# Kernel tuning notes

Measured on AMD Instinct MI355X. Metric: run time of the kernel, lower is better.

Reference implementation:

```python
import jax, jax.numpy as jnp
import numpy as np

DIM = 1024
NUM_HEADS = 16
HEAD_DIM = DIM // NUM_HEADS
WINDOW = 1024
GATE_IN = 20
B, T = 2, 2048
ROPE_BASE = 10000.0


def setup_inputs() -> dict:
    key = jax.random.key(0)
    ks = jax.random.split(key, 12)
    s = 0.02
    x = jax.random.normal(ks[0], (B, T, DIM), dtype=jnp.float32)
    Wq = jax.random.normal(ks[1], (DIM, DIM), dtype=jnp.float32) * s
    bq = jnp.zeros((DIM,), jnp.float32)
    Wk = jax.random.normal(ks[2], (DIM, DIM), dtype=jnp.float32) * s
    bk = jnp.zeros((DIM,), jnp.float32)
    Wv = jax.random.normal(ks[3], (DIM, DIM), dtype=jnp.float32) * s
    bv = jnp.zeros((DIM,), jnp.float32)
    # o_lin.weight is zero-initialized in the original; use random here so the
    # reference output/grads are non-degenerate.
    Wo = jax.random.normal(ks[4], (DIM, DIM), dtype=jnp.float32) * s
    bo = jnp.zeros((DIM,), jnp.float32)
    Wg = jax.random.normal(ks[5], (NUM_HEADS, GATE_IN), dtype=jnp.float32) * s
    bg = jnp.zeros((NUM_HEADS,), jnp.float32)
    # rotary tables, half-dim convention
    inv_freq = 1.0 / (ROPE_BASE ** (jnp.arange(0, HEAD_DIM, 2, dtype=jnp.float32) / HEAD_DIM))
    t = jnp.arange(T, dtype=jnp.float32)
    freqs = jnp.outer(t, inv_freq)  # [T, HEAD_DIM/2]
    return {"x": x, "Wq": Wq, "bq": bq, "Wk": Wk, "bk": bk, "Wv": Wv, "bv": bv,
            "Wo": Wo, "bo": bo, "Wg": Wg, "bg": bg,
            "cos": jnp.cos(freqs), "sin": jnp.sin(freqs)}


def _rope(u, cos, sin):
    # u: [B,T,H,hd]; cos/sin: [T, hd/2]
    u1, u2 = jnp.split(u, 2, axis=-1)
    c = cos[None, :, None, :]
    s = sin[None, :, None, :]
    return jnp.concatenate([u1 * c - u2 * s, u1 * s + u2 * c], axis=-1)


def reference(x, Wq, bq, Wk, bk, Wv, bv, Wo, bo, Wg, bg, cos, sin):
    Bx, Tx, D = x.shape
    q = (x @ Wq.T + bq).reshape(Bx, Tx, NUM_HEADS, HEAD_DIM)
    k = (x @ Wk.T + bk).reshape(Bx, Tx, NUM_HEADS, HEAD_DIM)
    v = (x @ Wv.T + bv).reshape(Bx, Tx, NUM_HEADS, HEAD_DIM)
    q = _rope(q, cos, sin)
    k = _rope(k, cos, sin)
    scale = 1.0 / jnp.sqrt(jnp.float32(HEAD_DIM))
    scores = jnp.einsum('bqhd,bkhd->bhqk', q, k) * scale  # [B,H,T,T]
    i = jnp.arange(Tx)[:, None]
    j = jnp.arange(Tx)[None, :]
    mask = (j <= i) & (j >= i - WINDOW)  # causal + sliding window (WINDOW left, 0 right)
    scores = jnp.where(mask[None, None], scores, jnp.float32(-1e30))
    probs = jax.nn.softmax(scores, axis=-1)
    o = jnp.einsum('bhqk,bkhd->bqhd', probs, v)  # [B,T,H,hd]
    gate = jax.nn.sigmoid(x[..., :GATE_IN] @ Wg.T + bg)  # [B,T,H]
    o = o * gate[..., None]
    o = o.reshape(Bx, Tx, D)
    return o @ Wo.T + bo
```

## Files before the change

### kernel.cpp

```cpp
#include <hip/hip_runtime.h>

#define DIMM 1024
#define NHEADS 16
#define HDIM 64
#define WIN 1024
#define GATEIN 20
#define BB 2
#define TT 2048
#define MTOT (BB*TT)

typedef __attribute__((ext_vector_type(8))) short short8;
typedef __attribute__((ext_vector_type(4))) float f32x4;
typedef __attribute__((ext_vector_type(16))) float f32x16;
typedef const __attribute__((address_space(1))) void gvoid_t;
typedef __attribute__((address_space(3))) void lvoid_t;

__device__ __forceinline__ unsigned short f2b(float f) {
  union { float f; unsigned u; } c; c.f = f;
  unsigned u = c.u + 0x7fffu + ((c.u >> 16) & 1u);
  return (unsigned short)(u >> 16);
}
__device__ __forceinline__ float b2f(unsigned short s) {
  union { unsigned u; float f; } c; c.u = ((unsigned)s) << 16;
  return c.f;
}
__device__ __forceinline__ unsigned cvt_pk_bf16(float lo, float hi) {
  unsigned r;
  asm("v_cvt_pk_bf16_f32 %0, %1, %2" : "=v"(r) : "v"(lo), "v"(hi));
  return r;
}
__device__ __forceinline__ float max3f(float a, float b, float c) {
  return fmaxf(fmaxf(a, b), c);
}
__device__ __forceinline__ float xmax32(float x) {
  union { float f; unsigned u; } c; c.f = x;
  auto pr = __builtin_amdgcn_permlane32_swap(c.u, c.u, false, false);
  union { unsigned u; float f; } a, b; a.u = pr[0]; b.u = pr[1];
  return fmaxf(a.f, b.f);
}
__device__ __forceinline__ float xsum32(float x) {
  union { float f; unsigned u; } c; c.f = x;
  auto pr = __builtin_amdgcn_permlane32_swap(c.u, c.u, false, false);
  union { unsigned u; float f; } a, b; a.u = pr[0]; b.u = pr[1];
  return a.f + b.f;
}

#define QSCALE (0.125f * 1.4426950408889634f)

__global__ void prep_kernel(const float* __restrict__ x,  const float* __restrict__ Wq,
                            const float* __restrict__ Wk, const float* __restrict__ Wv,
                            const float* __restrict__ Wo, const float* __restrict__ bq,
                            const float* __restrict__ bk, const float* __restrict__ bv,
                            unsigned short* __restrict__ xb, unsigned short* __restrict__ wqkv,
                            unsigned short* __restrict__ wob, float* __restrict__ bcat) {
  int i = blockIdx.x * blockDim.x + threadIdx.x;
  const float* src; unsigned short* dst; int off;
  if (i < 1048576)      { src = x;  dst = xb;             off = i; }
  else if (i < 1310720) { src = Wq; dst = wqkv;           off = i - 1048576; }
  else if (i < 1572864) { src = Wk; dst = wqkv + 1048576; off = i - 1310720; }
  else if (i < 1835008) { src = Wv; dst = wqkv + 2097152; off = i - 1572864; }
  else if (i < 2097152) { src = Wo; dst = wob;            off = i - 1835008; }
  else {
    int j = i - 2097152;
    if (j < 768) {
      const float* bsrc = (j < 256) ? bq : (j < 512) ? bk : bv;
      int bo = (j & 255) * 4;
      int db = (j < 256) ? 0 : (j < 512) ? 1024 : 2048;
      *(float4*)(bcat + db + bo) = *(const float4*)(bsrc + bo);
    }
    return;
  }
  float4 v = ((const float4*)src)[off];
  union { unsigned short s[4]; uint2 u; } o;
  o.s[0] = f2b(v.x); o.s[1] = f2b(v.y); o.s[2] = f2b(v.z); o.s[3] = f2b(v.w);
  *(uint2*)(dst + (size_t)off * 4) = o.u;
}

__global__ void gate_kernel(const float* __restrict__ x, const float* __restrict__ Wg,
                            const float* __restrict__ bg, float* __restrict__ gate) {
  int i = blockIdx.x * blockDim.x + threadIdx.x;
  if (i >= MTOT * NHEADS) return;
  int h = i & 15;
  int m = i >> 4;
  const float* xr = x + (size_t)m * DIMM;
  const float* wr = Wg + h * GATEIN;
  float z = bg[h];
#pragma unroll
  for (int g = 0; g < GATEIN; ++g) z += xr[g] * wr[g];
  gate[i] = 1.f / (1.f + __expf(-z));
}

__global__ __launch_bounds__(256) void gemm_qkv(const unsigned short* __restrict__ A,
                                                const unsigned short* __restrict__ Bw,
                                                const float* __restrict__ bias,
                                                const float* __restrict__ cosb,
                                                const float* __restrict__ sinb,
                                                unsigned short* __restrict__ qr,
                                                unsigned short* __restrict__ kr,
                                                unsigned short* __restrict__ vt) {
  const int K = DIMM, N = 3072;
  __shared__ __align__(16) unsigned short As[2][128 * 32];
  __shared__ __align__(16) unsigned short Bs[2][128 * 32];
  const int tid = threadIdx.x;
  const int lane = tid & 63, wid = tid >> 6;
  const int g = lane >> 4, r16 = lane & 15;

  const int fid = blockIdx.y * 24 + blockIdx.x;
  const int xcd = fid & 7;
  const int j = fid >> 3;
  const int m0 = (j & 31) * 128;
  const int n0 = (xcd * 3 + (j >> 5)) * 128;

  const int wr = (wid >> 1) * 64, wc = (wid & 1) * 64;
  const int wbase = wid * 64;

  int oaf[4], obf[4];
#pragma unroll
  for (int mf = 0; mf < 4; ++mf) {
    int row = wr + mf * 16 + r16;
    oaf[mf] = row * 32 + ((g ^ ((row >> 1) & 3)) * 8);
  }
#pragma unroll
  for (int nf = 0; nf < 4; ++nf) {
    int row = wc + nf * 16 + r16;
    obf[nf] = row * 32 + ((g ^ ((row >> 1) & 3)) * 8);
  }

  f32x4 acc[4][4];
#pragma unroll
  for (int i = 0; i < 4; ++i)
#pragma unroll
    for (int j2 = 0; j2 < 4; ++j2) acc[i][j2] = (f32x4){0.f, 0.f, 0.f, 0.f};

  auto stage = [&](int buf, int k0) {
#pragma unroll
    for (int jj = 0; jj < 2; ++jj) {
      int sbase = jj * 256 + wbase;
      int s = sbase + lane;
      int l = s ^ ((s >> 3) & 3);
      const unsigned short* gA = A + (size_t)(m0 + (l >> 2)) * K + k0 + (l & 3) * 8;
      __builtin_amdgcn_global_load_lds((gvoid_t*)gA,
          (lvoid_t*)((char*)&As[buf][0] + sbase * 16), 16, 0, 0);
      const unsigned short* gB = Bw + (size_t)(n0 + (l >> 2)) * K + k0 + (l & 3) * 8;
      __builtin_amdgcn_global_load_lds((gvoid_t*)gB,
          (lvoid_t*)((char*)&Bs[buf][0] + sbase * 16), 16, 0, 0);
    }
  };

  const int NT = K >> 5;
  stage(0, 0);
  __syncthreads();
  for (int t = 0; t < NT; ++t) {
    const int buf = t & 1;
    if (t + 1 < NT) stage(buf ^ 1, (t + 1) << 5);
    short8 af[4], bf[4];
#pragma unroll
    for (int mf = 0; mf < 4; ++mf) af[mf] = *(const short8*)(&As[buf][0] + oaf[mf]);
#pragma unroll
    for (int nf = 0; nf < 4; ++nf)  bf[nf] = *(const short8*)(&Bs[buf][0] + obf[nf]);
#pragma unroll
    for (int mf = 0; mf < 4; ++mf)
#pragma unroll
      for (int nf = 0; nf < 4; ++nf)
        acc[mf][nf] = __builtin_amdgcn_mfma_f32_16x16x32_bf16(af[mf], bf[nf], acc[mf][nf], 0, 0, 0);
    __syncthreads();
  }

  const int ncol = n0 + wc;
  const int seg  = ncol >> 10;
  const int h    = (ncol >> 6) & 15;
  const int bb   = m0 >> 11;
  const int tb   = (m0 + wr) & 2047;
  const size_t base = (size_t)(bb * NHEADS + h) * TT * HDIM;
  float bias_v[4];
#pragma unroll
  for (int nf = 0; nf < 4; ++nf) bias_v[nf] = bias[ncol + nf * 16 + r16];

  if (seg == 2) {
#pragma unroll
    for (int mf = 0; mf < 4; ++mf) {
      int kvt = (tb >> 5) + (mf >> 1);
#pragma unroll
      for (int nf = 0; nf < 4; ++nf) {
        union { unsigned short s4[4]; uint2 u; } w;
#pragma unroll
        for (int rr = 0; rr < 4; ++rr) w.s4[rr] = f2b(acc[mf][nf][rr] + bias_v[nf]);
        size_t addr = base + (size_t)kvt * 2048
                    + (size_t)((nf >> 1) * 2 + (mf & 1)) * 512
                    + (size_t)(g >> 1) * 256
                    + (size_t)((nf & 1) * 16 + r16) * 8 + 4 * (g & 1);
        *(uint2*)(vt + addr) = w.u;
      }
    }
  } else {
#pragma unroll
    for (int mf = 0; mf < 4; ++mf) {
#pragma unroll
      for (int rr = 0; rr < 4; ++rr) {
        int t = tb + mf * 16 + g * 4 + rr;
#pragma unroll
        for (int nf = 0; nf < 2; ++nf) {
          int d = nf * 16 + r16;
          float c = cosb[t * 32 + d], s = sinb[t * 32 + d];
          float v1 = acc[mf][nf][rr]     + bias_v[nf];
          float v2 = acc[mf][nf + 2][rr] + bias_v[nf + 2];
          float o1 = v1 * c - v2 * s;
          float o2 = v1 * s + v2 * c;
          if (seg == 0) {
            qr[base + (size_t)t * HDIM + d]      = f2b(o1 * QSCALE);
            qr[base + (size_t)t * HDIM + d + 32] = f2b(o2 * QSCALE);
          } else {
            size_t ok = base + (size_t)(t >> 5) * 2048 + (size_t)nf * 512
                      + (size_t)(r16 >> 3) * 256 + (size_t)(t & 31) * 8 + (r16 & 7);
            kr[ok]        = f2b(o1);
            kr[ok + 1024] = f2b(o2);
          }
        }
      }
    }
  }
}

template<int MF>
__global__ __launch_bounds__(256) void gemm_bt(const unsigned short* __restrict__ A,
                                               const unsigned short* __restrict__ Bw,
                                               const float* __restrict__ bias,
                                               float* __restrict__ Cout,
                                               int M, int N, int K) {
  __shared__ __align__(16) unsigned short As[2][MF * 32 * 32];
  __shared__ __align__(16) unsigned short Bs[2][128 * 32];
  const int tid = threadIdx.x;
  const int lane = tid & 63, wid = tid >> 6;
  const int g = lane >> 4, r16 = lane & 15;
  const int m0 = blockIdx.y * (MF * 32), n0 = blockIdx.x * 128;
  const int wr = (wid >> 1) * (MF * 16), wc = (wid & 1) * 64;
  const int wbase = wid * 64;

  int oaf[MF], obf[4];
#pragma unroll
  for (int mf = 0; mf < MF; ++mf) {
    int row = wr + mf * 16 + r16;
    oaf[mf] = row * 32 + ((g ^ ((row >> 1) & 3)) * 8);
  }
#pragma unroll
  for (int nf = 0; nf < 4; ++nf) {
    int row = wc + nf * 16 + r16;
    obf[nf] = row * 32 + ((g ^ ((row >> 1) & 3)) * 8);
  }

  f32x4 acc[MF][4];
#pragma unroll
  for (int i = 0; i < MF; ++i)
#pragma unroll
    for (int j = 0; j < 4; ++j) acc[i][j] = (f32x4){0.f, 0.f, 0.f, 0.f};

  auto stage = [&](int buf, int k0) {
#pragma unroll
    for (int j = 0; j < MF / 2; ++j) {
      int sbase = j * 256 + wbase;
      int s = sbase + lane;
      int l = s ^ ((s >> 3) & 3);
      const unsigned short* gA = A + (size_t)(m0 + (l >> 2)) * K + k0 + (l & 3) * 8;
      __builtin_amdgcn_global_load_lds((gvoid_t*)gA,
          (lvoid_t*)((char*)&As[buf][0] + sbase * 16), 16, 0, 0);
    }
#pragma unroll
    for (int j = 0; j < 2; ++j) {
      int sbase = j * 256 + wbase;
      int s = sbase + lane;
      int l = s ^ ((s >> 3) & 3);
      const unsigned short* gB = Bw + (size_t)(n0 + (l >> 2)) * K + k0 + (l & 3) * 8;
      __builtin_amdgcn_global_load_lds((gvoid_t*)gB,
          (lvoid_t*)((char*)&Bs[buf][0] + sbase * 16), 16, 0, 0);
    }
  };

  const int NT = K >> 5;
  stage(0, 0);
  __syncthreads();
  for (int t = 0; t < NT; ++t) {
    const int buf = t & 1;
    if (t + 1 < NT) stage(buf ^ 1, (t + 1) << 5);
    short8 af[MF], bf[4];
#pragma unroll
    for (int mf = 0; mf < MF; ++mf) af[mf] = *(const short8*)(&As[buf][0] + oaf[mf]);
#pragma unroll
    for (int nf = 0; nf < 4; ++nf)  bf[nf] = *(const short8*)(&Bs[buf][0] + obf[nf]);
#pragma unroll
    for (int mf = 0; mf < MF; ++mf)
#pragma unroll
      for (int nf = 0; nf < 4; ++nf)
        acc[mf][nf] = __builtin_amdgcn_mfma_f32_16x16x32_bf16(af[mf], bf[nf], acc[mf][nf], 0, 0, 0);
    __syncthreads();
  }
#pragma unroll
  for (int mf = 0; mf < MF; ++mf)
#pragma unroll
    for (int nf = 0; nf < 4; ++nf)
#pragma unroll
      for (int rr = 0; rr < 4; ++rr) {
        int m = m0 + wr + mf * 16 + g * 4 + rr;
        int n = n0 + wc + nf * 16 + r16;
        Cout[(size_t)m * N + n] = acc[mf][nf][rr] + bias[n];
      }
}

__global__ __launch_bounds__(256, 4) void attn_kernel(const unsigned short* __restrict__ qr,
                                                      const unsigned short* __restrict__ kr,
                                                      const unsigned short* __restrict__ vt,
                                                      const float* __restrict__ gate,
                                                      unsigned short* __restrict__ attn_out) {
  __shared__ float lds_m[4][32];
  __shared__ float lds_l[4][32];
  __shared__ float lds_O[3][64][33];
  const int tid = threadIdx.x;
  const int lane = tid & 63, wid = tid >> 6;
  const int l31 = lane & 31, hi = lane >> 5;

  const int fid = blockIdx.x;
  const int idx = fid >> 3;
  const int bh = (fid & 7) * 4 + (idx & 3);
  const int qt = 63 - (idx >> 2);
  const int q0 = qt * 32;
  const int b = bh >> 4, h = bh & 15;
  const unsigned short* kptr = kr + (size_t)bh * TT * HDIM;
  const unsigned short* vptr = vt + (size_t)bh * TT * HDIM;
  const int q = q0 + l31;

  short8 qf[4];
#pragma unroll
  for (int st = 0; st < 4; ++st)
    qf[st] = *(const short8*)(qr + (size_t)bh * TT * HDIM + (size_t)q * HDIM + st * 16 + hi * 8);

  f32x16 o0, o1;
#pragma unroll
  for (int r = 0; r < 16; ++r) { o0[r] = 0.f; o1[r] = 0.f; }
  float mrun = -1e30f, lrun = 0.f;

  int kv_lo = q0 - WIN;
  if (kv_lo < 0) kv_lo = 0;
  const int kv_hi = q0 + 32;

  for (int kv = kv_lo + wid * 32; kv < kv_hi; kv += 128) {
    const unsigned short* kf = kptr + (size_t)kv * 64 + lane * 8;
    short8 k0 = *(const short8*)(kf);
    short8 k1 = *(const short8*)(kf + 512);
    short8 k2 = *(const short8*)(kf + 1024);
    short8 k3 = *(const short8*)(kf + 1536);

    f32x16 s;
#pragma unroll
    for (int r = 0; r < 16; ++r) s[r] = 0.f;
    s = __builtin_amdgcn_mfma_f32_32x32x16_bf16(k0, qf[0], s, 0, 0, 0);
    s = __builtin_amdgcn_mfma_f32_32x32x16_bf16(k1, qf[1], s, 0, 0, 0);
    s = __builtin_amdgcn_mfma_f32_32x32x16_bf16(k2, qf[2], s, 0, 0, 0);
    s = __builtin_amdgcn_mfma_f32_32x32x16_bf16(k3, qf[3], s, 0, 0, 0);

    if (kv == q0) {
#pragma unroll
      for (int r = 0; r < 16; ++r) {
        int key = kv + (r & 3) + 8 * (r >> 2) + 4 * hi;
        s[r] = (key <= q) ? s[r] : -1e30f;
      }
    } else if (q0 >= WIN && kv == kv_lo) {
#pragma unroll
      for (int r = 0; r < 16; ++r) {
        int key = kv + (r & 3) + 8 * (r >> 2) + 4 * hi;
        s[r] = (key + WIN >= q) ? s[r] : -1e30f;
      }
    }

    float t0 = max3f(s[0],  s[1],  s[2]);
    float t1 = max3f(s[3],  s[4],  s[5]);
    float t2 = max3f(s[6],  s[7],  s[8]);
    float t3 = max3f(s[9],  s[10], s[11]);
    float t4 = max3f(s[12], s[13], s[14]);
    float lm = fmaxf(max3f(t0, t1, t2), max3f(t3, t4, s[15]));
    lm = xmax32(lm);

    if (!__all(lm - mrun <= 8.f)) {
      float mnew = fmaxf(mrun, lm);
      float scf = __builtin_exp2f(mrun - mnew);
      mrun = mnew;
      lrun *= scf;
#pragma unroll
      for (int r = 0; r < 16; ++r) { o0[r] *= scf; o1[r] *= scf; }
    }

#pragma unroll
    for (int r = 0; r < 16; ++r) s[r] = __builtin_exp2f(s[r] - mrun);

    float c0 = (s[0] + s[1]) + (s[2] + s[3]);
    float c1 = (s[4] + s[5]) + (s[6] + s[7]);
    float c2 = (s[8] + s[9]) + (s[10] + s[11]);
    float c3 = (s[12] + s[13]) + (s[14] + s[15]);
    lrun += xsum32((c0 + c1) + (c2 + c3));

    unsigned w0 = cvt_pk_bf16(s[0],  s[1]),  w1 = cvt_pk_bf16(s[2],  s[3]);
    unsigned w2 = cvt_pk_bf16(s[4],  s[5]),  w3 = cvt_pk_bf16(s[6],  s[7]);
    unsigned w4 = cvt_pk_bf16(s[8],  s[9]),  w5 = cvt_pk_bf16(s[10], s[11]);
    unsigned w6 = cvt_pk_bf16(s[12], s[13]), w7 = cvt_pk_bf16(s[14], s[15]);
    auto s1p = __builtin_amdgcn_permlane32_swap(w0, w2, false, false);
    auto s2p = __builtin_amdgcn_permlane32_swap(w1, w3, false, false);
    auto s3p = __builtin_amdgcn_permlane32_swap(w4, w6, false, false);
    auto s4p = __builtin_amdgcn_permlane32_swap(w5, w7, false, false);
    union { unsigned u[4]; short8 s8; } pf0, pf1;
    pf0.u[0] = s1p[0]; pf0.u[1] = s2p[0]; pf0.u[2] = s1p[1]; pf0.u[3] = s2p[1];
    pf1.u[0] = s3p[0]; pf1.u[1] = s4p[0]; pf1.u[2] = s3p[1]; pf1.u[3] = s4p[1];

    const unsigned short* vf = vptr + (size_t)kv * 64 + lane * 8;
    short8 vf00 = *(const short8*)(vf);
    short8 vf01 = *(const short8*)(vf + 512);
    short8 vf10 = *(const short8*)(vf + 1024);
    short8 vf11 = *(const short8*)(vf + 1536);

    o0 = __builtin_amdgcn_mfma_f32_32x32x16_bf16(vf00, pf0.s8, o0, 0, 0, 0);
    o1 = __builtin_amdgcn_mfma_f32_32x32x16_bf16(vf10, pf0.s8, o1, 0, 0, 0);
    o0 = __builtin_amdgcn_mfma_f32_32x32x16_bf16(vf01, pf1.s8, o0, 0, 0, 0);
    o1 = __builtin_amdgcn_mfma_f32_32x32x16_bf16(vf11, pf1.s8, o1, 0, 0, 0);
  }

  if (hi == 0) { lds_m[wid][l31] = mrun; lds_l[wid][l31] = lrun; }
  __syncthreads();
  float m0 = lds_m[0][l31], m1 = lds_m[1][l31], m2 = lds_m[2][l31], m3 = lds_m[3][l31];
  float mstar = fmaxf(fmaxf(m0, m1), fmaxf(m2, m3));
  float myscale = __builtin_exp2f(mrun - mstar);
  if (wid != 0) {
#pragma unroll
    for (int r = 0; r < 16; ++r) {
      lds_O[wid - 1][lane][r]      = o0[r] * myscale;
      lds_O[wid - 1][lane][16 + r] = o1[r] * myscale;
    }
  }
  __syncthreads();
  if (wid == 0) {
    float lstar = __builtin_exp2f(m0 - mstar) * lds_l[0][l31]
                + __builtin_exp2f(m1 - mstar) * lds_l[1][l31]
                + __builtin_exp2f(m2 - mstar) * lds_l[2][l31]
                + __builtin_exp2f(m3 - mstar) * lds_l[3][l31];
    float gv = gate[((size_t)b * TT + q) * NHEADS + h];
    float inv = gv / lstar;
    float of0[16], of1[16];
#pragma unroll
    for (int r = 0; r < 16; ++r) {
      of0[r] = o0[r] * myscale + lds_O[0][lane][r]      + lds_O[1][lane][r]      + lds_O[2][lane][r];
      of1[r] = o1[r] * myscale + lds_O[0][lane][16 + r] + lds_O[1][lane][16 + r] + lds_O[2][lane][16 + r];
    }
    unsigned short* orow = attn_out + ((size_t)b * TT + q) * DIMM + h * HDIM;
#pragma unroll
    for (int a2 = 0; a2 < 4; ++a2) {
      int d0 = a2 * 8 + hi * 4;
      union { unsigned short s[4]; uint2 u; } x0, x1;
#pragma unroll
      for (int c = 0; c < 4; ++c) {
        x0.s[c] = f2b(of0[a2 * 4 + c] * inv);
        x1.s[c] = f2b(of1[a2 * 4 + c] * inv);
      }
      *(uint2*)(orow + d0) = x0.u;
      *(uint2*)(orow + 32 + d0) = x1.u;
    }
  }
}

#define OFF_XB    ((size_t)0)
#define OFF_WQKV  ((size_t)8388608)
#define OFF_WO    ((size_t)14680064)
#define OFF_BCAT  ((size_t)16777216)
#define OFF_QR    ((size_t)41959424)
#define OFF_KR    ((size_t)50348032)
#define OFF_VT    ((size_t)58736640)
#define OFF_ATTN  ((size_t)67125248)
#define OFF_GATE  ((size_t)75513856)

extern "C" void kernel_launch(void* const* d_in, const int* in_sizes, int n_in,
                              void* d_out, int out_size, void* d_ws, size_t ws_size,
                              hipStream_t stream) {
  const float* x    = (const float*)d_in[0];
  const float* Wq   = (const float*)d_in[1];
  const float* bq   = (const float*)d_in[2];
  const float* Wk   = (const float*)d_in[3];
  const float* bk   = (const float*)d_in[4];
  const float* Wv   = (const float*)d_in[5];
  const float* bv   = (const float*)d_in[6];
  const float* Wo   = (const float*)d_in[7];
  const float* bo   = (const float*)d_in[8];
  const float* Wg   = (const float*)d_in[9];
  const float* bg   = (const float*)d_in[10];
  const float* cosb = (const float*)d_in[11];
  const float* sinb = (const float*)d_in[12];
  float* out = (float*)d_out;
  char* ws = (char*)d_ws;

  unsigned short* xb    = (unsigned short*)(ws + OFF_XB);
  unsigned short* wqkv  = (unsigned short*)(ws + OFF_WQKV);
  unsigned short* wob   = (unsigned short*)(ws + OFF_WO);
  float*          bcat  = (float*)(ws + OFF_BCAT);
  unsigned short* q_r   = (unsigned short*)(ws + OFF_QR);
  unsigned short* k_r   = (unsigned short*)(ws + OFF_KR);
  unsigned short* v_t   = (unsigned short*)(ws + OFF_VT);
  unsigned short* attn  = (unsigned short*)(ws + OFF_ATTN);
  float*          gateb = (float*)(ws + OFF_GATE);

  prep_kernel<<<8195, 256, 0, stream>>>(x, Wq, Wk, Wv, Wo, bq, bk, bv, xb, wqkv, wob, bcat);
  gate_kernel<<<256, 256, 0, stream>>>(x, Wg, bg, gateb);

  gemm_qkv<<<dim3(24, 32), 256, 0, stream>>>(xb, wqkv, bcat, cosb, sinb, q_r, k_r, v_t);

  attn_kernel<<<2048, 256, 0, stream>>>(q_r, k_r, v_t, gateb, attn);

  gemm_bt<2><<<dim3(8, 64), 256, 0, stream>>>(attn, wob, bo, out, MTOT, 1024, 1024);
}
```

Before: 107.3 us.

## Split attention KV range across eight waves and drop QKV GEMM XCD swizzle

The attention kernel now launches 512 threads per block, so eight waves each take every eighth 32-key chunk of the window instead of four. The cross-wave softmax merge and LDS output reduction are widened to match, which shortens each wave's serial KV loop at the cost of more LDS and a larger final reduction done by wave 0 alone. Separately, the QKV GEMM drops its XCD-aware block remapping and uses plain blockIdx tile coordinates, which may change L2 locality across chiplets.

New measurement: 115.7 us. +7.9%, slower.

```diff
diff --git a/kernel.cpp b/kernel.cpp
--- a/kernel.cpp
+++ b/kernel.cpp
@@ -98,19 +98,13 @@
                                                 unsigned short* __restrict__ qr,
                                                 unsigned short* __restrict__ kr,
                                                 unsigned short* __restrict__ vt) {
-  const int K = DIMM, N = 3072;
+  const int K = DIMM;
   __shared__ __align__(16) unsigned short As[2][128 * 32];
   __shared__ __align__(16) unsigned short Bs[2][128 * 32];
   const int tid = threadIdx.x;
   const int lane = tid & 63, wid = tid >> 6;
   const int g = lane >> 4, r16 = lane & 15;
-
-  const int fid = blockIdx.y * 24 + blockIdx.x;
-  const int xcd = fid & 7;
-  const int j = fid >> 3;
-  const int m0 = (j & 31) * 128;
-  const int n0 = (xcd * 3 + (j >> 5)) * 128;
-
+  const int m0 = blockIdx.y * 128, n0 = blockIdx.x * 128;
   const int wr = (wid >> 1) * 64, wc = (wid & 1) * 64;
   const int wbase = wid * 64;
 
@@ -305,14 +299,14 @@
       }
 }
 
-__global__ __launch_bounds__(256, 4) void attn_kernel(const unsigned short* __restrict__ qr,
+__global__ __launch_bounds__(512, 4) void attn_kernel(const unsigned short* __restrict__ qr,
                                                       const unsigned short* __restrict__ kr,
                                                       const unsigned short* __restrict__ vt,
                                                       const float* __restrict__ gate,
                                                       unsigned short* __restrict__ attn_out) {
-  __shared__ float lds_m[4][32];
-  __shared__ float lds_l[4][32];
-  __shared__ float lds_O[3][64][33];
+  __shared__ float lds_m[8][32];
+  __shared__ float lds_l[8][32];
+  __shared__ float lds_O[7][64][33];
   const int tid = threadIdx.x;
   const int lane = tid & 63, wid = tid >> 6;
   const int l31 = lane & 31, hi = lane >> 5;
@@ -341,7 +335,7 @@
   if (kv_lo < 0) kv_lo = 0;
   const int kv_hi = q0 + 32;
 
-  for (int kv = kv_lo + wid * 32; kv < kv_hi; kv += 128) {
+  for (int kv = kv_lo + wid * 32; kv < kv_hi; kv += 256) {
     const unsigned short* kf = kptr + (size_t)kv * 64 + lane * 8;
     short8 k0 = *(const short8*)(kf);
     short8 k1 = *(const short8*)(kf + 512);
@@ -422,8 +416,9 @@
 
   if (hi == 0) { lds_m[wid][l31] = mrun; lds_l[wid][l31] = lrun; }
   __syncthreads();
-  float m0 = lds_m[0][l31], m1 = lds_m[1][l31], m2 = lds_m[2][l31], m3 = lds_m[3][l31];
-  float mstar = fmaxf(fmaxf(m0, m1), fmaxf(m2, m3));
+  float mstar = -1e30f;
+#pragma unroll
+  for (int w = 0; w < 8; ++w) mstar = fmaxf(mstar, lds_m[w][l31]);
   float myscale = __builtin_exp2f(mrun - mstar);
   if (wid != 0) {
 #pragma unroll
@@ -434,17 +429,22 @@
   }
   __syncthreads();
   if (wid == 0) {
-    float lstar = __builtin_exp2f(m0 - mstar) * lds_l[0][l31]
-                + __builtin_exp2f(m1 - mstar) * lds_l[1][l31]
-                + __builtin_exp2f(m2 - mstar) * lds_l[2][l31]
-                + __builtin_exp2f(m3 - mstar) * lds_l[3][l31];
+    float lstar = 0.f;
+#pragma unroll
+    for (int w = 0; w < 8; ++w)
+      lstar += __builtin_exp2f(lds_m[w][l31] - mstar) * lds_l[w][l31];
     float gv = gate[((size_t)b * TT + q) * NHEADS + h];
     float inv = gv / lstar;
     float of0[16], of1[16];
 #pragma unroll
     for (int r = 0; r < 16; ++r) {
-      of0[r] = o0[r] * myscale + lds_O[0][lane][r]      + lds_O[1][lane][r]      + lds_O[2][lane][r];
-      of1[r] = o1[r] * myscale + lds_O[0][lane][16 + r] + lds_O[1][lane][16 + r] + lds_O[2][lane][16 + r];
+      float a0 = o0[r] * myscale, a1 = o1[r] * myscale;
+#pragma unroll
+      for (int w = 0; w < 7; ++w) {
+        a0 += lds_O[w][lane][r];
+        a1 += lds_O[w][lane][16 + r];
+      }
+      of0[r] = a0; of1[r] = a1;
     }
     unsigned short* orow = attn_out + ((size_t)b * TT + q) * DIMM + h * HDIM;
 #pragma unroll
@@ -506,7 +506,7 @@
 
   gemm_qkv<<<dim3(24, 32), 256, 0, stream>>>(xb, wqkv, bcat, cosb, sinb, q_r, k_r, v_t);
 
-  attn_kernel<<<2048, 256, 0, stream>>>(q_r, k_r, v_t, gateb, attn);
+  attn_kernel<<<2048, 512, 0, stream>>>(q_r, k_r, v_t, gateb, attn);
 
   gemm_bt<2><<<dim3(8, 64), 256, 0, stream>>>(attn, wob, bo, out, MTOT, 1024, 1024);
 }
```
